# Optimization experiments

Hardware: AMD Instinct MI355X
Metric: run time of the kernel (lower is better)

The kernel has to match this reference:

```python
import jax, jax.numpy as jnp
import numpy as np

N = 200000
C = 128
VOX = 0.05
EPS = 1e-5
OFFSETS = np.array([[dz, dy, dx] for dz in (-1, 0, 1) for dy in (-1, 0, 1) for dx in (-1, 0, 1)], dtype=np.int64)


def setup_inputs() -> dict:
    key = jax.random.key(0)
    ks = jax.random.split(key, 8)
    gp = jax.random.normal(ks[0], (N, 14), jnp.float32)
    # ---- voxelization tables (int constants, computed once in numpy) ----
    pts = np.asarray(gp[:, :3], dtype=np.float64)
    vc = np.floor(pts / VOX).astype(np.int64)
    vc = vc - vc.min(axis=0)
    mx = vc.max(axis=0) + 1
    h = vc[:, 0] * mx[1] * mx[2] + vc[:, 1] * mx[2] + vc[:, 2]
    uh, inv = np.unique(h, return_inverse=True)
    M = int(uh.shape[0])
    vcoord = np.zeros((M, 3), np.int64)
    vcoord[inv] = vc  # coords identical for same hash
    nbr_idx = np.zeros((M, 27), np.int32)
    nbr_mask = np.zeros((M, 27), np.float32)
    for o in range(27):
        nc = vcoord + OFFSETS[o]
        inb = (nc >= 0).all(1) & (nc < mx).all(1)
        nh = nc[:, 0] * mx[1] * mx[2] + nc[:, 1] * mx[2] + nc[:, 2]
        pos = np.clip(np.searchsorted(uh, nh), 0, M - 1)
        found = inb & (uh[pos] == nh)
        nbr_idx[:, o] = np.where(found, pos, 0)
        nbr_mask[:, o] = found.astype(np.float32)
    s = 0.05
    return {
        'gaussian_params': gp,
        'w_enc': jax.random.normal(ks[1], (14, C), jnp.float32) * s,
        'b_enc': jnp.zeros((C,), jnp.float32),
        'ln_g': jnp.ones((C,), jnp.float32),
        'ln_b': jnp.zeros((C,), jnp.float32),
        'conv_w': jax.random.normal(ks[2], (4, 27, C, C), jnp.float32) * s,
        'bn_g': jnp.ones((4, C), jnp.float32),
        'bn_b': jnp.zeros((4, C), jnp.float32),
        'w1': jax.random.normal(ks[3], (C, C // 2), jnp.float32) * s,
        'b1': jnp.zeros((C // 2,), jnp.float32),
        'w2': jax.random.normal(ks[4], (C // 2, 14), jnp.float32) * s,
        'b2': jnp.zeros((14,), jnp.float32),
        'nbr_mask': jnp.asarray(nbr_mask),
        'inv_idx': jnp.asarray(inv.astype(np.int32)),
        'nbr_idx': jnp.asarray(nbr_idx),
        'num_voxels': M,
    }


def _bn(x, g, b):
    m = x.mean(0)
    v = x.var(0)
    return (x - m) * jax.lax.rsqrt(v + EPS) * g + b


def _subm(x, W, nbr_idx, nbr_mask):
    # submanifold 3x3x3 conv: sum over 27 offsets of masked neighbor gather @ W[o]
    out = jnp.zeros_like(x)
    for o in range(27):
        out = out + (x[nbr_idx[:, o]] * nbr_mask[:, o:o + 1]) @ W[o]
    return out


def _forward(gp, w_enc, b_enc, ln_g, ln_b, conv_w, bn_g, bn_b, w1, b1, w2, b2, nbr_mask, inv_idx, nbr_idx, num_voxels):
    # input encoder: Linear -> LayerNorm -> ReLU
    f = gp @ w_enc + b_enc
    mu = f.mean(-1, keepdims=True)
    var = f.var(-1, keepdims=True)
    f = jax.nn.relu((f - mu) * jax.lax.rsqrt(var + EPS) * ln_g + ln_b)
    # points -> voxels: segment mean (the op the torch code did with a Python loop)
    cnt = jax.ops.segment_sum(jnp.ones((gp.shape[0],), f.dtype), inv_idx, num_segments=num_voxels)
    x = jax.ops.segment_sum(f, inv_idx, num_segments=num_voxels) / cnt[:, None]
    # 2 residual sparse conv blocks (BN uses batch stats, training-mode forward)
    for blk in range(2):
        idn = x
        out = _subm(x, conv_w[2 * blk], nbr_idx, nbr_mask)
        out = jax.nn.relu(_bn(out, bn_g[2 * blk], bn_b[2 * blk]))
        out = _subm(out, conv_w[2 * blk + 1], nbr_idx, nbr_mask)
        x = jax.nn.relu(_bn(out, bn_g[2 * blk + 1], bn_b[2 * blk + 1]) + idn)
    # voxels -> points, output head, residual add
    pf = x[inv_idx]
    delta = jax.nn.relu(pf @ w1 + b1) @ w2 + b2
    return gp[:, :14] + delta


def reference(gaussian_params, w_enc, b_enc, ln_g, ln_b, conv_w, bn_g, bn_b, w1, b1, w2, b2, nbr_mask, inv_idx, nbr_idx, num_voxels):
    return _forward(gaussian_params, w_enc, b_enc, ln_g, ln_b, conv_w, bn_g, bn_b, w1, b1, w2, b2, nbr_mask, inv_idx, nbr_idx, num_voxels)
```

## Files before the change

### kernel.cpp

```cpp
#include <hip/hip_runtime.h>

typedef __bf16 bf16x8 __attribute__((ext_vector_type(8)));
typedef float f32x16 __attribute__((ext_vector_type(16)));

#define LN_EPS 1e-5f
#define AS1 __attribute__((address_space(1)))
#define AS3 __attribute__((address_space(3)))

__device__ __forceinline__ unsigned f2bf_rne(float f) {
    unsigned x = __float_as_uint(f);
    return (x + 0x7fffu + ((x >> 16) & 1u)) >> 16;
}

__device__ __forceinline__ float bf2f(unsigned short u) {
    return __uint_as_float((unsigned)u << 16);
}

__global__ void pack_w_kernel(const float* __restrict__ cw, unsigned short* __restrict__ Wp, int E) {
    int idx = blockIdx.x * 256 + threadIdx.x;
    if (idx >= E) return;
    float v = cw[idx];
    int n  = idx & 127;
    int c  = (idx >> 7) & 127;
    int oc = idx >> 14;
    Wp[oc * 16384 + (c >> 3) * 1024 + n * 8 + (c & 7)] = (unsigned short)f2bf_rne(v);
}

__global__ void pack_w1_kernel(const float* __restrict__ w1, unsigned short* __restrict__ Wp1) {
    int idx = blockIdx.x * 256 + threadIdx.x;
    if (idx >= 8192) return;
    int k = idx >> 6, n = idx & 63;
    Wp1[(k >> 3) * 512 + n * 8 + (k & 7)] = (unsigned short)f2bf_rne(w1[k * 64 + n]);
}

__global__ void prep_nbr_kernel(const int* __restrict__ nbr_idx, const float* __restrict__ nbr_mask,
                                int* __restrict__ T, unsigned* __restrict__ act, int M) {
    int m = blockIdx.x * 256 + threadIdx.x;
    if (m >= M) return;
    unsigned bits = 0;
#pragma unroll
    for (int o = 0; o < 27; ++o) {
        bool f = nbr_mask[m * 27 + o] != 0.f;
        int g = f ? nbr_idx[m * 27 + o] : M;
        T[o * M + m] = g;
        bits |= (f ? 1u : 0u) << o;
    }
    atomicOr(&act[m >> 7], bits);
}

__global__ __launch_bounds__(256) void encode_kernel(
    const float* __restrict__ gp, const float* __restrict__ w_enc,
    const float* __restrict__ b_enc, const float* __restrict__ ln_g,
    const float* __restrict__ ln_b, const int* __restrict__ inv_idx,
    float* __restrict__ vsum, float* __restrict__ cnt, int N)
{
    int p = blockIdx.x * 4 + (threadIdx.x >> 6);
    int lane = threadIdx.x & 63;
    if (p >= N) return;
    float gv[14];
#pragma unroll
    for (int i = 0; i < 14; ++i) gv[i] = gp[p * 14 + i];
    float f0 = b_enc[lane], f1 = b_enc[lane + 64];
#pragma unroll
    for (int i = 0; i < 14; ++i) {
        f0 = fmaf(gv[i], w_enc[i * 128 + lane], f0);
        f1 = fmaf(gv[i], w_enc[i * 128 + lane + 64], f1);
    }
    float s = f0 + f1;
#pragma unroll
    for (int off = 32; off; off >>= 1) s += __shfl_xor(s, off);
    float mean = s * 0.0078125f;
    float d0 = f0 - mean, d1 = f1 - mean;
    float v = d0 * d0 + d1 * d1;
#pragma unroll
    for (int off = 32; off; off >>= 1) v += __shfl_xor(v, off);
    float rs = rsqrtf(v * 0.0078125f + LN_EPS);
    float h0 = d0 * rs * ln_g[lane] + ln_b[lane];
    float h1 = d1 * rs * ln_g[lane + 64] + ln_b[lane + 64];
    h0 = h0 > 0.f ? h0 : 0.f;
    h1 = h1 > 0.f ? h1 : 0.f;
    int vx = inv_idx[p];
    atomicAdd(&vsum[vx * 128 + lane], h0);
    atomicAdd(&vsum[vx * 128 + lane + 64], h1);
    if (lane == 0) atomicAdd(&cnt[vx], 1.0f);
}

__global__ void vox_mean_kernel(const float* __restrict__ vsum, const float* __restrict__ cnt,
                                unsigned short* __restrict__ out, int total4) {
    int idx = blockIdx.x * 256 + threadIdx.x;
    if (idx >= total4) return;
    int e0 = idx * 4;
    float r = 1.f / cnt[e0 >> 7];
    float4 v = *(const float4*)(vsum + e0);
    uint2 pk;
    pk.x = f2bf_rne(v.x * r) | (f2bf_rne(v.y * r) << 16);
    pk.y = f2bf_rne(v.z * r) | (f2bf_rne(v.w * r) << 16);
    *(uint2*)(out + e0) = pk;
}

__global__ __launch_bounds__(256, 4) void subm_conv_kernel(
    const unsigned short* __restrict__ xin,
    const unsigned short* __restrict__ Wp,
    const int* __restrict__ T, const unsigned* __restrict__ act,
    float* __restrict__ yout, float* __restrict__ stats, int M)
{
    __shared__ uint4 Ws[2048];

    const int tid = threadIdx.x;
    const int lane = tid & 63;
    const int w = tid >> 6;
    const int m0 = blockIdx.x * 128;
    const int rw = w * 32;
    const int q = lane >> 5;
    const int l31 = lane & 31;
    int myrow = m0 + rw + l31;
    if (myrow >= M) myrow = M - 1;

    f32x16 acc[4];
#pragma unroll
    for (int t = 0; t < 4; ++t)
#pragma unroll
        for (int r = 0; r < 16; ++r) acc[t][r] = 0.f;

    const uint4* xin4 = (const uint4*)xin;
    unsigned amask = act[blockIdx.x];

    while (amask) {
        int o = __ffs(amask) - 1;
        amask &= amask - 1;

        __syncthreads();

        const uint4* WpO4 = (const uint4*)Wp + o * 2048;
#pragma unroll
        for (int rep = 0; rep < 8; ++rep) {
            __builtin_amdgcn_global_load_lds(
                (const AS1 unsigned int*)(WpO4 + rep * 256 + tid),
                (AS3 unsigned int*)(Ws + rep * 256 + w * 64), 16, 0, 0);
        }

        int g = T[o * M + myrow];
        uint4 af[8];
#pragma unroll
        for (int j = 0; j < 8; ++j) af[j] = xin4[g * 16 + 2 * j + q];

        __syncthreads();

#pragma unroll
        for (int ks = 0; ks < 8; ++ks) {
            int kb = (ks << 1) | q;
            bf16x8 a = *(const bf16x8*)&af[ks];
#pragma unroll
            for (int tn = 0; tn < 4; ++tn) {
                bf16x8 b = ((const bf16x8*)Ws)[kb * 128 + tn * 32 + l31];
                acc[tn] = __builtin_amdgcn_mfma_f32_32x32x16_bf16(a, b, acc[tn], 0, 0, 0);
            }
        }
    }

#pragma unroll
    for (int tn = 0; tn < 4; ++tn) {
        int col = tn * 32 + l31;
        float s = 0.f, sq = 0.f;
#pragma unroll
        for (int r = 0; r < 16; ++r) {
            int rloc = (r & 3) + 8 * (r >> 2) + 4 * q + rw;
            int grow = m0 + rloc;
            float v = acc[tn][r];
            if (grow < M) yout[grow * 128 + col] = v;
            s += v; sq += v * v;
        }
        s += __shfl_xor(s, 32);
        sq += __shfl_xor(sq, 32);
        if (lane < 32) {
            atomicAdd(&stats[col], s);
            atomicAdd(&stats[128 + col], sq);
        }
    }
}

__global__ void bn_relu_kernel(const float* __restrict__ y, const float* __restrict__ stats,
                               const float* __restrict__ g, const float* __restrict__ b,
                               unsigned short* __restrict__ out, int total4, float invM) {
    int idx = blockIdx.x * 256 + threadIdx.x;
    if (idx >= total4) return;
    int e0 = idx * 4;
    int c0 = e0 & 127;
    float4 yv = *(const float4*)(y + e0);
    float h[4];
    const float* yp = (const float*)&yv;
#pragma unroll
    for (int j = 0; j < 4; ++j) {
        int c = c0 + j;
        float mean = stats[c] * invM;
        float var = stats[128 + c] * invM - mean * mean;
        float sc = g[c] * rsqrtf(var + LN_EPS);
        float sh = b[c] - mean * sc;
        float vv = yp[j] * sc + sh;
        h[j] = vv > 0.f ? vv : 0.f;
    }
    uint2 pk;
    pk.x = f2bf_rne(h[0]) | (f2bf_rne(h[1]) << 16);
    pk.y = f2bf_rne(h[2]) | (f2bf_rne(h[3]) << 16);
    *(uint2*)(out + e0) = pk;
}

__global__ void bn_relu_res_kernel(const float* __restrict__ y, const float* __restrict__ stats,
                                   const float* __restrict__ g, const float* __restrict__ b,
                                   const unsigned short* __restrict__ idn,
                                   unsigned short* __restrict__ out, int total4, float invM) {
    int idx = blockIdx.x * 256 + threadIdx.x;
    if (idx >= total4) return;
    int e0 = idx * 4;
    int c0 = e0 & 127;
    float4 yv = *(const float4*)(y + e0);
    uint2 iv = *(const uint2*)(idn + e0);
    float id[4];
    id[0] = __uint_as_float(iv.x << 16);
    id[1] = __uint_as_float(iv.x & 0xffff0000u);
    id[2] = __uint_as_float(iv.y << 16);
    id[3] = __uint_as_float(iv.y & 0xffff0000u);
    float h[4];
    const float* yp = (const float*)&yv;
#pragma unroll
    for (int j = 0; j < 4; ++j) {
        int c = c0 + j;
        float mean = stats[c] * invM;
        float var = stats[128 + c] * invM - mean * mean;
        float sc = g[c] * rsqrtf(var + LN_EPS);
        float sh = b[c] - mean * sc;
        float vv = yp[j] * sc + sh + id[j];
        h[j] = vv > 0.f ? vv : 0.f;
    }
    uint2 pk;
    pk.x = f2bf_rne(h[0]) | (f2bf_rne(h[1]) << 16);
    pk.y = f2bf_rne(h[2]) | (f2bf_rne(h[3]) << 16);
    *(uint2*)(out + e0) = pk;
}

__global__ __launch_bounds__(256) void head_vox_kernel(
    const unsigned short* __restrict__ A,
    const unsigned short* __restrict__ Wp1,
    const float* __restrict__ b1, const float* __restrict__ w2,
    const float* __restrict__ b2, float* __restrict__ Dv, int M)
{
    __shared__ uint4 W1s[1024];
    __shared__ unsigned short Hs[8192];
    __shared__ float w2s[896];

    const int tid = threadIdx.x;
    const int lane = tid & 63;
    const int w = tid >> 6;
    const int m0 = blockIdx.x * 128;
    const int rw = w * 32;
    const int q = lane >> 5;
    const int l31 = lane & 31;
    int myrow = m0 + rw + l31;
    if (myrow > M) myrow = M;

#pragma unroll
    for (int rep = 0; rep < 4; ++rep) {
        __builtin_amdgcn_global_load_lds(
            (const AS1 unsigned int*)((const uint4*)Wp1 + rep * 256 + tid),
            (AS3 unsigned int*)(W1s + rep * 256 + w * 64), 16, 0, 0);
    }
    for (int i = tid; i < 896; i += 256) w2s[i] = w2[i];

    const uint4* xin4 = (const uint4*)A;
    uint4 af[8];
#pragma unroll
    for (int j = 0; j < 8; ++j) af[j] = xin4[myrow * 16 + 2 * j + q];

    f32x16 acc[2];
#pragma unroll
    for (int t = 0; t < 2; ++t)
#pragma unroll
        for (int r = 0; r < 16; ++r) acc[t][r] = 0.f;

    __syncthreads();

#pragma unroll
    for (int ks = 0; ks < 8; ++ks) {
        int kb = (ks << 1) | q;
        bf16x8 a = *(const bf16x8*)&af[ks];
#pragma unroll
        for (int tn = 0; tn < 2; ++tn) {
            bf16x8 b = ((const bf16x8*)W1s)[kb * 64 + tn * 32 + l31];
            acc[tn] = __builtin_amdgcn_mfma_f32_32x32x16_bf16(a, b, acc[tn], 0, 0, 0);
        }
    }

#pragma unroll
    for (int tn = 0; tn < 2; ++tn) {
        int col = tn * 32 + l31;
        float bias = b1[col];
        int ch = col >> 3, ce = col & 7;
#pragma unroll
        for (int r = 0; r < 16; ++r) {
            int rloc = (r & 3) + 8 * (r >> 2) + 4 * q + rw;
            float v = acc[tn][r] + bias;
            v = v > 0.f ? v : 0.f;
            Hs[rloc * 64 + (ch ^ (rloc & 7)) * 8 + ce] = (unsigned short)f2bf_rne(v);
        }
    }
    __syncthreads();

    int r2 = tid >> 1;
    int c0 = (tid & 1) * 7;
    float o[7];
#pragma unroll
    for (int j = 0; j < 7; ++j) o[j] = b2[c0 + j];
#pragma unroll
    for (int c = 0; c < 8; ++c) {
        bf16x8 hv = ((const bf16x8*)Hs)[r2 * 8 + (c ^ (r2 & 7))];
#pragma unroll
        for (int e = 0; e < 8; ++e) {
            float h = bf2f(((const unsigned short*)&hv)[e]);
            int k = c * 8 + e;
#pragma unroll
            for (int j = 0; j < 7; ++j) o[j] = fmaf(h, w2s[k * 14 + c0 + j], o[j]);
        }
    }
    int grow = m0 + r2;
    if (grow < M) {
#pragma unroll
        for (int j = 0; j < 7; ++j) Dv[grow * 14 + c0 + j] = o[j];
    }
}

__global__ void head_scatter_kernel(const float* __restrict__ gp, const float* __restrict__ Dv,
                                    const int* __restrict__ inv_idx, float* __restrict__ out, int N) {
    int p = blockIdx.x * 256 + threadIdx.x;
    if (p >= N) return;
    int vx = inv_idx[p];
#pragma unroll
    for (int c = 0; c < 14; ++c) out[p * 14 + c] = gp[p * 14 + c] + Dv[vx * 14 + c];
}

extern "C" void kernel_launch(void* const* d_in, const int* in_sizes, int n_in,
                              void* d_out, int out_size, void* d_ws, size_t ws_size,
                              hipStream_t stream) {
    const float* gp       = (const float*)d_in[0];
    const float* w_enc    = (const float*)d_in[1];
    const float* b_enc    = (const float*)d_in[2];
    const float* ln_g     = (const float*)d_in[3];
    const float* ln_b     = (const float*)d_in[4];
    const float* conv_w   = (const float*)d_in[5];
    const float* bn_g     = (const float*)d_in[6];
    const float* bn_b     = (const float*)d_in[7];
    const float* w1       = (const float*)d_in[8];
    const float* b1       = (const float*)d_in[9];
    const float* w2       = (const float*)d_in[10];
    const float* b2       = (const float*)d_in[11];
    const float* nbr_mask = (const float*)d_in[12];
    const int*   inv_idx  = (const int*)d_in[13];
    const int*   nbr_idx  = (const int*)d_in[14];

    const int N = in_sizes[0] / 14;
    const int M = in_sizes[12] / 27;
    const int ntiles = (M + 127) / 128;

    char* ws = (char*)d_ws;
    size_t off = 0;
    unsigned short* Wp = (unsigned short*)(ws + off); off += (size_t)4 * 27 * 16384 * 2;
    unsigned short* A  = (unsigned short*)(ws + off); off += (size_t)(M + 1) * 128 * 2;
    unsigned short* H  = (unsigned short*)(ws + off); off += (size_t)(M + 1) * 128 * 2;
    float* Yraw  = (float*)(ws + off);
    size_t zoff = off;
    off += (size_t)M * 128 * 4;
    float* cnt   = (float*)(ws + off); off += (size_t)M * 4;
    float* stats = (float*)(ws + off); off += 4 * 256 * 4;
    unsigned* act = (unsigned*)(ws + off); off += (size_t)ntiles * 4;
    size_t zbytes = off - zoff;
    int* T = (int*)(ws + off); off += (size_t)27 * M * 4;
    unsigned short* Wp1 = (unsigned short*)(ws + off); off += 8192 * 2;
    float* Dv = Yraw;

    hipMemsetAsync(Yraw, 0, zbytes, stream);
    hipMemsetAsync(A + (size_t)M * 128, 0, 256, stream);
    hipMemsetAsync(H + (size_t)M * 128, 0, 256, stream);

    const int E = 4 * 27 * 128 * 128;
    pack_w_kernel<<<(E + 255) / 256, 256, 0, stream>>>(conv_w, Wp, E);
    pack_w1_kernel<<<32, 256, 0, stream>>>(w1, Wp1);
    prep_nbr_kernel<<<(M + 255) / 256, 256, 0, stream>>>(nbr_idx, nbr_mask, T, act, M);
    encode_kernel<<<(N + 3) / 4, 256, 0, stream>>>(gp, w_enc, b_enc, ln_g, ln_b, inv_idx, Yraw, cnt, N);
    const int total4 = M * 32;
    vox_mean_kernel<<<(total4 + 255) / 256, 256, 0, stream>>>(Yraw, cnt, A, total4);

    const float invM = 1.f / (float)M;
    for (int blk = 0; blk < 2; ++blk) {
        int c0 = 2 * blk, c1 = 2 * blk + 1;
        subm_conv_kernel<<<ntiles, 256, 0, stream>>>(
            A, Wp + (size_t)c0 * 27 * 16384, T, act, Yraw, stats + c0 * 256, M);
        bn_relu_kernel<<<(total4 + 255) / 256, 256, 0, stream>>>(
            Yraw, stats + c0 * 256, bn_g + c0 * 128, bn_b + c0 * 128, H, total4, invM);
        subm_conv_kernel<<<ntiles, 256, 0, stream>>>(
            H, Wp + (size_t)c1 * 27 * 16384, T, act, Yraw, stats + c1 * 256, M);
        bn_relu_res_kernel<<<(total4 + 255) / 256, 256, 0, stream>>>(
            Yraw, stats + c1 * 256, bn_g + c1 * 128, bn_b + c1 * 128, A, A, total4, invM);
    }
    head_vox_kernel<<<ntiles, 256, 0, stream>>>(A, Wp1, b1, w2, b2, Dv, M);
    head_scatter_kernel<<<(N + 255) / 256, 256, 0, stream>>>(gp, Dv, inv_idx, (float*)d_out, N);
}
```

Before: 1.524 ms.

## Replace atomic voxel scatter with CSR gather and double-buffer conv weights

Point-to-voxel averaging no longer scatters with float atomics. A count, two-level scan and fill pass build a per-voxel point list, and a gather kernel then encodes and averages each voxel's points, writing bf16 directly. The sparse conv now uses 512-thread blocks over 256-row tiles and double-buffers the per-offset weight tile in LDS, so the next offset's weights load while the current one computes. This adds several small kernel launches, and the larger tiles mean fewer blocks with a looser active-offset mask per tile, which can bring in more empty offsets.

```diff
diff --git a/kernel.cpp b/kernel.cpp
--- a/kernel.cpp
+++ b/kernel.cpp
@@ -45,71 +45,138 @@
         T[o * M + m] = g;
         bits |= (f ? 1u : 0u) << o;
     }
-    atomicOr(&act[m >> 7], bits);
-}
-
-__global__ __launch_bounds__(256) void encode_kernel(
+    atomicOr(&act[m >> 8], bits);
+}
+
+__global__ void count_kernel(const int* __restrict__ inv, int* __restrict__ cnt, int N) {
+    int p = blockIdx.x * 256 + threadIdx.x;
+    if (p < N) atomicAdd(&cnt[inv[p]], 1);
+}
+
+__global__ void scan1_kernel(const int* __restrict__ cnt, int* __restrict__ starts,
+                             int* __restrict__ partials, int M) {
+    __shared__ int sdata[256];
+    int t = threadIdx.x;
+    int base = blockIdx.x * 1024;
+    int v[4], tot = 0;
+#pragma unroll
+    for (int j = 0; j < 4; ++j) {
+        int idx = base + t * 4 + j;
+        v[j] = idx < M ? cnt[idx] : 0;
+        tot += v[j];
+    }
+    sdata[t] = tot;
+    __syncthreads();
+    for (int off = 1; off < 256; off <<= 1) {
+        int x = (t >= off) ? sdata[t - off] : 0;
+        __syncthreads();
+        sdata[t] += x;
+        __syncthreads();
+    }
+    int run = sdata[t] - tot;
+#pragma unroll
+    for (int j = 0; j < 4; ++j) {
+        int idx = base + t * 4 + j;
+        if (idx < M) starts[idx] = run;
+        run += v[j];
+    }
+    if (t == 255) partials[blockIdx.x] = run;
+}
+
+__global__ void scan2_kernel(int* __restrict__ partials, int nb) {
+    __shared__ int sdata[256];
+    int t = threadIdx.x;
+    int v[4], tot = 0;
+#pragma unroll
+    for (int j = 0; j < 4; ++j) {
+        int idx = t * 4 + j;
+        v[j] = idx < nb ? partials[idx] : 0;
+        tot += v[j];
+    }
+    sdata[t] = tot;
+    __syncthreads();
+    for (int off = 1; off < 256; off <<= 1) {
+        int x = (t >= off) ? sdata[t - off] : 0;
+        __syncthreads();
+        sdata[t] += x;
+        __syncthreads();
+    }
+    int run = sdata[t] - tot;
+#pragma unroll
+    for (int j = 0; j < 4; ++j) {
+        int idx = t * 4 + j;
+        if (idx < nb) partials[idx] = run;
+        run += v[j];
+    }
+}
+
+__global__ void fill_kernel(const int* __restrict__ inv, const int* __restrict__ starts,
+                            const int* __restrict__ partials, int* __restrict__ tmp,
+                            int* __restrict__ plist, int N) {
+    int p = blockIdx.x * 256 + threadIdx.x;
+    if (p >= N) return;
+    int v = inv[p];
+    int slot = atomicAdd(&tmp[v], 1);
+    plist[starts[v] + partials[v >> 10] + slot] = p;
+}
+
+__global__ __launch_bounds__(256) void vox_encode_kernel(
     const float* __restrict__ gp, const float* __restrict__ w_enc,
     const float* __restrict__ b_enc, const float* __restrict__ ln_g,
-    const float* __restrict__ ln_b, const int* __restrict__ inv_idx,
-    float* __restrict__ vsum, float* __restrict__ cnt, int N)
+    const float* __restrict__ ln_b, const int* __restrict__ starts,
+    const int* __restrict__ partials, const int* __restrict__ cnt,
+    const int* __restrict__ plist, unsigned short* __restrict__ A, int M)
 {
-    int p = blockIdx.x * 4 + (threadIdx.x >> 6);
+    int v = blockIdx.x * 4 + (threadIdx.x >> 6);
     int lane = threadIdx.x & 63;
-    if (p >= N) return;
-    float gv[14];
-#pragma unroll
-    for (int i = 0; i < 14; ++i) gv[i] = gp[p * 14 + i];
-    float f0 = b_enc[lane], f1 = b_enc[lane + 64];
-#pragma unroll
-    for (int i = 0; i < 14; ++i) {
-        f0 = fmaf(gv[i], w_enc[i * 128 + lane], f0);
-        f1 = fmaf(gv[i], w_enc[i * 128 + lane + 64], f1);
-    }
-    float s = f0 + f1;
-#pragma unroll
-    for (int off = 32; off; off >>= 1) s += __shfl_xor(s, off);
-    float mean = s * 0.0078125f;
-    float d0 = f0 - mean, d1 = f1 - mean;
-    float v = d0 * d0 + d1 * d1;
-#pragma unroll
-    for (int off = 32; off; off >>= 1) v += __shfl_xor(v, off);
-    float rs = rsqrtf(v * 0.0078125f + LN_EPS);
-    float h0 = d0 * rs * ln_g[lane] + ln_b[lane];
-    float h1 = d1 * rs * ln_g[lane + 64] + ln_b[lane + 64];
-    h0 = h0 > 0.f ? h0 : 0.f;
-    h1 = h1 > 0.f ? h1 : 0.f;
-    int vx = inv_idx[p];
-    atomicAdd(&vsum[vx * 128 + lane], h0);
-    atomicAdd(&vsum[vx * 128 + lane + 64], h1);
-    if (lane == 0) atomicAdd(&cnt[vx], 1.0f);
-}
-
-__global__ void vox_mean_kernel(const float* __restrict__ vsum, const float* __restrict__ cnt,
-                                unsigned short* __restrict__ out, int total4) {
-    int idx = blockIdx.x * 256 + threadIdx.x;
-    if (idx >= total4) return;
-    int e0 = idx * 4;
-    float r = 1.f / cnt[e0 >> 7];
-    float4 v = *(const float4*)(vsum + e0);
-    uint2 pk;
-    pk.x = f2bf_rne(v.x * r) | (f2bf_rne(v.y * r) << 16);
-    pk.y = f2bf_rne(v.z * r) | (f2bf_rne(v.w * r) << 16);
-    *(uint2*)(out + e0) = pk;
-}
-
-__global__ __launch_bounds__(256, 4) void subm_conv_kernel(
+    if (v >= M) return;
+    int st = starts[v] + partials[v >> 10];
+    int n = cnt[v];
+    const float2* w2p = (const float2*)w_enc;
+    float2 be = ((const float2*)b_enc)[lane];
+    float2 lg = ((const float2*)ln_g)[lane];
+    float2 lb = ((const float2*)ln_b)[lane];
+    float a0 = 0.f, a1 = 0.f;
+    for (int i = 0; i < n; ++i) {
+        int p = plist[st + i];
+        float f0 = be.x, f1 = be.y;
+#pragma unroll
+        for (int k = 0; k < 14; ++k) {
+            float gv = gp[p * 14 + k];
+            float2 wv = w2p[k * 64 + lane];
+            f0 = fmaf(gv, wv.x, f0);
+            f1 = fmaf(gv, wv.y, f1);
+        }
+        float s = f0 + f1;
+#pragma unroll
+        for (int off = 32; off; off >>= 1) s += __shfl_xor(s, off);
+        float mean = s * 0.0078125f;
+        float d0 = f0 - mean, d1 = f1 - mean;
+        float var = d0 * d0 + d1 * d1;
+#pragma unroll
+        for (int off = 32; off; off >>= 1) var += __shfl_xor(var, off);
+        float rs = rsqrtf(var * 0.0078125f + LN_EPS);
+        float h0 = d0 * rs * lg.x + lb.x;
+        float h1 = d1 * rs * lg.y + lb.y;
+        a0 += h0 > 0.f ? h0 : 0.f;
+        a1 += h1 > 0.f ? h1 : 0.f;
+    }
+    float r = 1.f / (float)n;
+    ((unsigned*)A)[v * 64 + lane] = f2bf_rne(a0 * r) | (f2bf_rne(a1 * r) << 16);
+}
+
+__global__ __launch_bounds__(512, 4) void subm_conv_kernel(
     const unsigned short* __restrict__ xin,
     const unsigned short* __restrict__ Wp,
     const int* __restrict__ T, const unsigned* __restrict__ act,
     float* __restrict__ yout, float* __restrict__ stats, int M)
 {
-    __shared__ uint4 Ws[2048];
+    __shared__ uint4 Ws[2][2048];
 
     const int tid = threadIdx.x;
     const int lane = tid & 63;
     const int w = tid >> 6;
-    const int m0 = blockIdx.x * 128;
+    const int m0 = blockIdx.x * 256;
     const int rw = w * 32;
     const int q = lane >> 5;
     const int l31 = lane & 31;
@@ -125,37 +192,52 @@
     const uint4* xin4 = (const uint4*)xin;
     unsigned amask = act[blockIdx.x];
 
-    while (amask) {
-        int o = __ffs(amask) - 1;
-        amask &= amask - 1;
+    int o_cur = __ffs(amask) - 1;
+    amask &= amask - 1;
+
+    {
+        const uint4* WpO4 = (const uint4*)Wp + o_cur * 2048;
+#pragma unroll
+        for (int rep = 0; rep < 4; ++rep)
+            __builtin_amdgcn_global_load_lds(
+                (const AS1 unsigned int*)(WpO4 + rep * 512 + tid),
+                (AS3 unsigned int*)(&Ws[0][rep * 512 + w * 64]), 16, 0, 0);
+    }
+
+    int buf = 0;
+    while (o_cur >= 0) {
+        int o_next = -1;
+        if (amask) { o_next = __ffs(amask) - 1; amask &= amask - 1; }
+
+        int g = T[o_cur * M + myrow];
+        uint4 af[8];
+#pragma unroll
+        for (int j = 0; j < 8; ++j) af[j] = xin4[g * 16 + 2 * j + q];
 
         __syncthreads();
 
-        const uint4* WpO4 = (const uint4*)Wp + o * 2048;
-#pragma unroll
-        for (int rep = 0; rep < 8; ++rep) {
-            __builtin_amdgcn_global_load_lds(
-                (const AS1 unsigned int*)(WpO4 + rep * 256 + tid),
-                (AS3 unsigned int*)(Ws + rep * 256 + w * 64), 16, 0, 0);
-        }
-
-        int g = T[o * M + myrow];
-        uint4 af[8];
-#pragma unroll
-        for (int j = 0; j < 8; ++j) af[j] = xin4[g * 16 + 2 * j + q];
-
-        __syncthreads();
-
+        if (o_next >= 0) {
+            const uint4* WpO4 = (const uint4*)Wp + o_next * 2048;
+#pragma unroll
+            for (int rep = 0; rep < 4; ++rep)
+                __builtin_amdgcn_global_load_lds(
+                    (const AS1 unsigned int*)(WpO4 + rep * 512 + tid),
+                    (AS3 unsigned int*)(&Ws[buf ^ 1][rep * 512 + w * 64]), 16, 0, 0);
+        }
+
+        const bf16x8* wsb = (const bf16x8*)&Ws[buf][0];
 #pragma unroll
         for (int ks = 0; ks < 8; ++ks) {
             int kb = (ks << 1) | q;
             bf16x8 a = *(const bf16x8*)&af[ks];
 #pragma unroll
             for (int tn = 0; tn < 4; ++tn) {
-                bf16x8 b = ((const bf16x8*)Ws)[kb * 128 + tn * 32 + l31];
+                bf16x8 b = wsb[kb * 128 + tn * 32 + l31];
                 acc[tn] = __builtin_amdgcn_mfma_f32_32x32x16_bf16(a, b, acc[tn], 0, 0, 0);
             }
         }
+        buf ^= 1;
+        o_cur = o_next;
     }
 
 #pragma unroll
@@ -358,25 +440,30 @@
 
     const int N = in_sizes[0] / 14;
     const int M = in_sizes[12] / 27;
-    const int ntiles = (M + 127) / 128;
+    const int ntiles256 = (M + 255) / 256;
+    const int ntiles128 = (M + 127) / 128;
+    const int nb = (M + 1023) / 1024;
 
     char* ws = (char*)d_ws;
     size_t off = 0;
-    unsigned short* Wp = (unsigned short*)(ws + off); off += (size_t)4 * 27 * 16384 * 2;
-    unsigned short* A  = (unsigned short*)(ws + off); off += (size_t)(M + 1) * 128 * 2;
-    unsigned short* H  = (unsigned short*)(ws + off); off += (size_t)(M + 1) * 128 * 2;
-    float* Yraw  = (float*)(ws + off);
+    unsigned short* Wp  = (unsigned short*)(ws + off); off += (size_t)4 * 27 * 16384 * 2;
+    unsigned short* Wp1 = (unsigned short*)(ws + off); off += 8192 * 2;
+    unsigned short* A   = (unsigned short*)(ws + off); off += (size_t)(M + 1) * 128 * 2;
+    unsigned short* H   = (unsigned short*)(ws + off); off += (size_t)(M + 1) * 128 * 2;
+    float* Yraw  = (float*)(ws + off); off += (size_t)M * 128 * 4;
+    int* T       = (int*)(ws + off); off += (size_t)27 * M * 4;
+    int* starts  = (int*)(ws + off); off += (size_t)M * 4;
+    int* plist   = (int*)(ws + off); off += (size_t)N * 4;
+    int* partials= (int*)(ws + off); off += 1024 * 4;
     size_t zoff = off;
-    off += (size_t)M * 128 * 4;
-    float* cnt   = (float*)(ws + off); off += (size_t)M * 4;
+    int* cnt     = (int*)(ws + off); off += (size_t)M * 4;
+    int* tmp     = (int*)(ws + off); off += (size_t)M * 4;
     float* stats = (float*)(ws + off); off += 4 * 256 * 4;
-    unsigned* act = (unsigned*)(ws + off); off += (size_t)ntiles * 4;
+    unsigned* act= (unsigned*)(ws + off); off += (size_t)ntiles256 * 4;
     size_t zbytes = off - zoff;
-    int* T = (int*)(ws + off); off += (size_t)27 * M * 4;
-    unsigned short* Wp1 = (unsigned short*)(ws + off); off += 8192 * 2;
     float* Dv = Yraw;
 
-    hipMemsetAsync(Yraw, 0, zbytes, stream);
+    hipMemsetAsync(cnt, 0, zbytes, stream);
     hipMemsetAsync(A + (size_t)M * 128, 0, 256, stream);
     hipMemsetAsync(H + (size_t)M * 128, 0, 256, stream);
 
@@ -384,22 +471,27 @@
     pack_w_kernel<<<(E + 255) / 256, 256, 0, stream>>>(conv_w, Wp, E);
     pack_w1_kernel<<<32, 256, 0, stream>>>(w1, Wp1);
     prep_nbr_kernel<<<(M + 255) / 256, 256, 0, stream>>>(nbr_idx, nbr_mask, T, act, M);
-    encode_kernel<<<(N + 3) / 4, 256, 0, stream>>>(gp, w_enc, b_enc, ln_g, ln_b, inv_idx, Yraw, cnt, N);
+
+    count_kernel<<<(N + 255) / 256, 256, 0, stream>>>(inv_idx, cnt, N);
+    scan1_kernel<<<nb, 256, 0, stream>>>(cnt, starts, partials, M);
+    scan2_kernel<<<1, 256, 0, stream>>>(partials, nb);
+    fill_kernel<<<(N + 255) / 256, 256, 0, stream>>>(inv_idx, starts, partials, tmp, plist, N);
+    vox_encode_kernel<<<(M + 3) / 4, 256, 0, stream>>>(
+        gp, w_enc, b_enc, ln_g, ln_b, starts, partials, cnt, plist, A, M);
+
     const int total4 = M * 32;
-    vox_mean_kernel<<<(total4 + 255) / 256, 256, 0, stream>>>(Yraw, cnt, A, total4);
-
     const float invM = 1.f / (float)M;
     for (int blk = 0; blk < 2; ++blk) {
         int c0 = 2 * blk, c1 = 2 * blk + 1;
-        subm_conv_kernel<<<ntiles, 256, 0, stream>>>(
+        subm_conv_kernel<<<ntiles256, 512, 0, stream>>>(
             A, Wp + (size_t)c0 * 27 * 16384, T, act, Yraw, stats + c0 * 256, M);
         bn_relu_kernel<<<(total4 + 255) / 256, 256, 0, stream>>>(
             Yraw, stats + c0 * 256, bn_g + c0 * 128, bn_b + c0 * 128, H, total4, invM);
-        subm_conv_kernel<<<ntiles, 256, 0, stream>>>(
+        subm_conv_kernel<<<ntiles256, 512, 0, stream>>>(
             H, Wp + (size_t)c1 * 27 * 16384, T, act, Yraw, stats + c1 * 256, M);
         bn_relu_res_kernel<<<(total4 + 255) / 256, 256, 0, stream>>>(
             Yraw, stats + c1 * 256, bn_g + c1 * 128, bn_b + c1 * 128, A, A, total4, invM);
     }
-    head_vox_kernel<<<ntiles, 256, 0, stream>>>(A, Wp1, b1, w2, b2, Dv, M);
+    head_vox_kernel<<<ntiles128, 256, 0, stream>>>(A, Wp1, b1, w2, b2, Dv, M);
     head_scatter_kernel<<<(N + 255) / 256, 256, 0, stream>>>(gp, Dv, inv_idx, (float*)d_out, N);
 }
```

New measurement: 1.740 ms. 14.2% more time.
